# Kernel tuning notes

Measured on AMD Instinct MI355X. Metric: run time of the kernel, lower is better.

The kernel has to match this reference:

```python
import jax, jax.numpy as jnp
import numpy as np


def _lstm_scan(xs, K, R, b, units):
    """Keras-style LSTM over time-major xs [T,B,F].
    Gate order i,f,g,o; recurrent_activation=sigmoid; activation=swish
    (applied to candidate g AND to cell state in h = o*swish(c))."""
    B = xs.shape[1]
    h0 = jnp.zeros((B, units), xs.dtype)
    c0 = jnp.zeros((B, units), xs.dtype)

    def step(carry, xt):
        h, c = carry
        z = xt @ K + h @ R + b  # [B, 4U]
        i, f, g, o = jnp.split(z, 4, axis=-1)
        i = jax.nn.sigmoid(i)
        f = jax.nn.sigmoid(f)
        g = jax.nn.swish(g)
        o = jax.nn.sigmoid(o)
        c = f * c + i * g
        h = o * jax.nn.swish(c)
        return (h, c), h

    _, hs = jax.lax.scan(step, (h0, c0), xs)
    return hs  # [T,B,U]


def setup_inputs() -> dict:
    B, T, F, U = 32, 512, 64, 512
    key = jax.random.key(0)
    ks = jax.random.split(key, 7)
    s = 0.05  # RandomUniform-ish small init scale
    x = jax.random.normal(ks[0], (B, T, F), jnp.float32)
    Kf = jax.random.uniform(ks[1], (F, 4 * U), jnp.float32, -s, s)
    Rf = jax.random.uniform(ks[2], (U, 4 * U), jnp.float32, -s, s)
    bf = jax.random.uniform(ks[3], (4 * U,), jnp.float32, -s, s)
    Kb = jax.random.uniform(ks[4], (F, 4 * U), jnp.float32, -s, s)
    Rb = jax.random.uniform(ks[5], (U, 4 * U), jnp.float32, -s, s)
    bb = jax.random.uniform(ks[6], (4 * U,), jnp.float32, -s, s)
    return {"x": x, "Kf": Kf, "Rf": Rf, "bf": bf, "Kb": Kb, "Rb": Rb, "bb": bb}


def reference(x, Kf, Rf, bf, Kb, Rb, bb):
    U = Rf.shape[0]
    xs = jnp.swapaxes(x, 0, 1)  # [T,B,F] time-major
    h_fwd = _lstm_scan(xs, Kf, Rf, bf, U)                      # [T,B,U]
    h_bwd = _lstm_scan(xs[::-1], Kb, Rb, bb, U)[::-1]          # [T,B,U]
    out = jnp.concatenate([h_fwd, h_bwd], axis=-1)             # [T,B,2U]
    return jnp.swapaxes(out, 0, 1)                              # [B,T,2U]
```

## Files before the change

kernel.cpp:

```cpp
#include <hip/hip_runtime.h>
#include <hip/hip_cooperative_groups.h>
#include <hip/hip_bf16.h>

namespace cg = cooperative_groups;

#define T_STEPS 512
#define BATCH   32
#define FDIM    64
#define UDIM    512
#define NWG_DIR 32

typedef __attribute__((ext_vector_type(8))) __bf16 bf16x8;
typedef __attribute__((ext_vector_type(4))) float  f32x4;


__global__ __launch_bounds__(512, 2)
void lstm_bidir_kernel(const float* __restrict__ x,
                       const float* __restrict__ Kf, const float* __restrict__ Rf,
                       const float* __restrict__ bfp,
                       const float* __restrict__ Kb, const float* __restrict__ Rb,
                       const float* __restrict__ bbp,
                       float* __restrict__ out, float* __restrict__ ws)
{
    __shared__ __align__(16) unsigned char hsb[BATCH * 1024];
    __shared__ __align__(16) unsigned char xsb[2][BATCH * 128];
    __shared__ __align__(16) float zbuf[BATCH * 68];
    __shared__ float cbuf[512];
    __shared__ float bsh[64];

    const int tid = threadIdx.x;
    const int wg  = blockIdx.x;
    const int dir   = wg >> 5;
    const int slice = wg & 31;
    const int colbase = slice * 16;

    const float* Kg = dir ? Kb : Kf;
    const float* Rg = dir ? Rb : Rf;
    const float* bg = dir ? bbp : bfp;

    unsigned char* wsb = (unsigned char*)ws;
    int* cnt = (int*)(wsb + 131072);

    {
        int g = wg * 512 + tid;
        if (g < 8192) {
            ((unsigned int*)wsb)[g] = 0u;
        } else if (g < 16384) {
            ((unsigned int*)wsb)[g + 8192] = 0u;
        } else if (g < 16384 + 2 * T_STEPS) {
            cnt[g - 16384] = 0;
        }
    }
    if (tid < 64) bsh[tid] = bg[(tid >> 4) * 512 + colbase + (tid & 15)];
    cbuf[tid] = 0.f;

    const int lane = tid & 63;
    const int w    = tid >> 6;
    const int mt   = w >> 2;
    const int gate = w & 3;
    const int bn   = lane & 15;
    const int kq   = lane >> 4;
    const int gcol = gate * 512 + colbase + bn;

    bf16x8 breg[18];
    #pragma unroll
    for (int s = 0; s < 16; ++s) {
        const int k0 = s * 32 + kq * 8;
        bf16x8 v;
        #pragma unroll
        for (int e = 0; e < 8; ++e)
            v[e] = (__bf16)Rg[(size_t)(k0 + e) * 2048 + gcol];
        breg[s] = v;
    }
    #pragma unroll
    for (int s = 0; s < 2; ++s) {
        const int k0 = s * 32 + kq * 8;
        bf16x8 v;
        #pragma unroll
        for (int e = 0; e < 8; ++e)
            v[e] = (__bf16)Kg[(size_t)(k0 + e) * 2048 + gcol];
        breg[16 + s] = v;
    }

    {
        const int t0 = dir ? (T_STEPS - 1) : 0;
        if (tid < 256) {
            int b = tid >> 3, m = tid & 7;
            const float4* xg = (const float4*)(x + (size_t)b * (T_STEPS * FDIM) + (size_t)t0 * FDIM + m * 8);
            float4 v0 = xg[0], v1 = xg[1];
            unsigned int p0 = ((unsigned int)__builtin_bit_cast(unsigned short, (__bf16)v0.x)) |
                              ((unsigned int)__builtin_bit_cast(unsigned short, (__bf16)v0.y) << 16);
            unsigned int p1 = ((unsigned int)__builtin_bit_cast(unsigned short, (__bf16)v0.z)) |
                              ((unsigned int)__builtin_bit_cast(unsigned short, (__bf16)v0.w) << 16);
            unsigned int p2 = ((unsigned int)__builtin_bit_cast(unsigned short, (__bf16)v1.x)) |
                              ((unsigned int)__builtin_bit_cast(unsigned short, (__bf16)v1.y) << 16);
            unsigned int p3 = ((unsigned int)__builtin_bit_cast(unsigned short, (__bf16)v1.z)) |
                              ((unsigned int)__builtin_bit_cast(unsigned short, (__bf16)v1.w) << 16);
            uint4 pk = make_uint4(p0, p1, p2, p3);
            *(uint4*)(xsb[0] + b * 128 + (m ^ (b & 7)) * 16) = pk;
        }
    }

    cg::grid_group grid = cg::this_grid();
    grid.sync();

    const int bb = tid >> 4;
    const int q  = tid & 15;
    float h_keep = 0.f;

    int p = 0;
    #pragma unroll 1
    for (int t = 0; t < T_STEPS; ++t) {
        if (t > 0) {
            const int txp = dir ? (T_STEPS - t) : (t - 1);
            out[(size_t)bb * (T_STEPS * 2 * UDIM) + (size_t)txp * (2 * UDIM)
                + dir * UDIM + colbase + q] = h_keep;
        }

        {
            const unsigned char* srcrow = wsb + (size_t)(dir * 2 + p) * 32768 + bb * 1024;
            const int inv = bb & 7;
            uint4 r0, r1, r2, r3;
            asm volatile("global_load_dwordx4 %0, %1, off sc0 sc1"
                         : "=&v"(r0) : "v"(srcrow + (q +  0) * 16) : "memory");
            asm volatile("global_load_dwordx4 %0, %1, off sc0 sc1"
                         : "=&v"(r1) : "v"(srcrow + (q + 16) * 16) : "memory");
            asm volatile("global_load_dwordx4 %0, %1, off sc0 sc1"
                         : "=&v"(r2) : "v"(srcrow + (q + 32) * 16) : "memory");
            asm volatile("global_load_dwordx4 %0, %1, off sc0 sc1"
                         : "=&v"(r3) : "v"(srcrow + (q + 48) * 16) : "memory");

            if (t + 1 < T_STEPS && tid < 256) {
                const int tn = dir ? (T_STEPS - 2 - t) : (t + 1);
                int b = tid >> 3, m = tid & 7;
                const float4* xg = (const float4*)(x + (size_t)b * (T_STEPS * FDIM) + (size_t)tn * FDIM + m * 8);
                float4 v0 = xg[0], v1 = xg[1];
                unsigned int p0 = ((unsigned int)__builtin_bit_cast(unsigned short, (__bf16)v0.x)) |
                                  ((unsigned int)__builtin_bit_cast(unsigned short, (__bf16)v0.y) << 16);
                unsigned int p1 = ((unsigned int)__builtin_bit_cast(unsigned short, (__bf16)v0.z)) |
                                  ((unsigned int)__builtin_bit_cast(unsigned short, (__bf16)v0.w) << 16);
                unsigned int p2 = ((unsigned int)__builtin_bit_cast(unsigned short, (__bf16)v1.x)) |
                                  ((unsigned int)__builtin_bit_cast(unsigned short, (__bf16)v1.y) << 16);
                unsigned int p3 = ((unsigned int)__builtin_bit_cast(unsigned short, (__bf16)v1.z)) |
                                  ((unsigned int)__builtin_bit_cast(unsigned short, (__bf16)v1.w) << 16);
                uint4 pk = make_uint4(p0, p1, p2, p3);
                *(uint4*)(xsb[(t + 1) & 1] + b * 128 + (m ^ (b & 7)) * 16) = pk;
            }

            asm volatile("s_waitcnt vmcnt(0)" ::: "memory");
            __builtin_amdgcn_sched_barrier(0);

            unsigned char* hrow = hsb + bb * 1024;
            *(uint4*)(hrow + (((q +  0) ^ inv) << 4)) = r0;
            *(uint4*)(hrow + (((q + 16) ^ inv) << 4)) = r1;
            *(uint4*)(hrow + (((q + 32) ^ inv) << 4)) = r2;
            *(uint4*)(hrow + (((q + 48) ^ inv) << 4)) = r3;
        }
        __syncthreads();

        f32x4 acc = {0.f, 0.f, 0.f, 0.f};
        {
            const int arow = mt * 16 + bn;
            const int inv  = arow & 7;
            const unsigned char* hrowA = hsb + arow * 1024;
            #pragma unroll
            for (int s = 0; s < 16; ++s) {
                int m = s * 4 + kq;
                bf16x8 a = *(const bf16x8*)(hrowA + ((m ^ inv) * 16));
                acc = __builtin_amdgcn_mfma_f32_16x16x32_bf16(a, breg[s], acc, 0, 0, 0);
            }
            const unsigned char* xrowA = xsb[t & 1] + arow * 128;
            #pragma unroll
            for (int s = 0; s < 2; ++s) {
                int m = s * 4 + kq;
                bf16x8 a = *(const bf16x8*)(xrowA + ((m ^ inv) * 16));
                acc = __builtin_amdgcn_mfma_f32_16x16x32_bf16(a, breg[16 + s], acc, 0, 0, 0);
            }
            const int zb = mt * 16 + kq * 4;
            #pragma unroll
            for (int j = 0; j < 4; ++j)
                zbuf[(zb + j) * 68 + gate * 16 + bn] = acc[j];
        }
        __syncthreads();

        {
            const float* zr = zbuf + bb * 68 + q;
            float zi = zr[0]  + bsh[q];
            float zf = zr[16] + bsh[16 + q];
            float zg = zr[32] + bsh[32 + q];
            float zo = zr[48] + bsh[48 + q];
            float gi = 1.f / (1.f + __expf(-zi));
            float gf = 1.f / (1.f + __expf(-zf));
            float gg = zg / (1.f + __expf(-zg));
            float go = 1.f / (1.f + __expf(-zo));
            float cv = gf * cbuf[tid] + gi * gg;
            cbuf[tid] = cv;
            float h  = go * (cv / (1.f + __expf(-cv)));
            h_keep = h;

            unsigned short hu = __builtin_bit_cast(unsigned short, (__bf16)h);
            int other = __shfl_xor((int)hu, 1);
            if ((q & 1) == 0) {
                unsigned int packed = (unsigned int)hu | ((unsigned int)(unsigned short)other << 16);
                unsigned int* dst = (unsigned int*)(wsb + (size_t)(dir * 2 + (p ^ 1)) * 32768);
                __hip_atomic_store(dst + bb * 256 + ((colbase + q) >> 1), packed,
                                   __ATOMIC_RELAXED, __HIP_MEMORY_SCOPE_AGENT);
            }
        }
        __syncthreads();

        if (t < T_STEPS - 1) {
            if (tid == 0) {
                asm volatile("s_waitcnt vmcnt(0)" ::: "memory");
                int* c0 = &cnt[dir * T_STEPS + t];
                __hip_atomic_fetch_add(c0, 1, __ATOMIC_RELAXED, __HIP_MEMORY_SCOPE_AGENT);
                while (__hip_atomic_load(c0, __ATOMIC_RELAXED, __HIP_MEMORY_SCOPE_AGENT) < NWG_DIR)
                    __builtin_amdgcn_s_sleep(1);
            }
            __syncthreads();
        }
        p ^= 1;
    }

    {
        const int txl = dir ? 0 : (T_STEPS - 1);
        out[(size_t)bb * (T_STEPS * 2 * UDIM) + (size_t)txl * (2 * UDIM)
            + dir * UDIM + colbase + q] = h_keep;
    }
}

extern "C" void kernel_launch(void* const* d_in, const int* in_sizes, int n_in,
                              void* d_out, int out_size, void* d_ws, size_t ws_size,
                              hipStream_t stream) {
    (void)in_sizes; (void)n_in; (void)out_size; (void)ws_size;
    const float* x  = (const float*)d_in[0];
    const float* Kf = (const float*)d_in[1];
    const float* Rf = (const float*)d_in[2];
    const float* bf = (const float*)d_in[3];
    const float* Kb = (const float*)d_in[4];
    const float* Rb = (const float*)d_in[5];
    const float* bb = (const float*)d_in[6];
    float* out = (float*)d_out;
    float* ws  = (float*)d_ws;

    void* args[] = {&x, &Kf, &Rf, &bf, &Kb, &Rb, &bb, &out, &ws};
    hipLaunchCooperativeKernel((const void*)lstm_bidir_kernel,
                               dim3(64), dim3(512), args, 0, stream);
}
```

Baseline: 1.580 ms.

## Replace per-step counter barrier with sentinel-flagged triple-buffered hidden state polling

Drops the per-timestep atomic counter barrier between the 32 workgroups of each direction. Instead, the hidden state lives in a three-slot ring buffer, and each slot is pre-filled with a 0xFFFFFFFF sentinel. Readers spin on the data itself until no sentinel remains, then reset their own columns of the slot two steps ahead to the sentinel. The x prefetch load is also issued before the polling loop so it overlaps. This removes a full block-wide syncthreads, the atomic round-trip and the sleep polling per step. The cost is repeated 4KB-per-row reloads while waiting, and correctness now relies on a bf16 pair never bit-matching the sentinel.

Result: faster. 1.453 ms (-8.0%).

```diff
diff --git a/kernel.cpp b/kernel.cpp
--- a/kernel.cpp
+++ b/kernel.cpp
@@ -9,6 +9,7 @@
 #define FDIM    64
 #define UDIM    512
 #define NWG_DIR 32
+#define SENT    0xFFFFFFFFu
 
 typedef __attribute__((ext_vector_type(8))) __bf16 bf16x8;
 typedef __attribute__((ext_vector_type(4))) float  f32x4;
@@ -39,17 +40,14 @@
     const float* bg = dir ? bbp : bfp;
 
     unsigned char* wsb = (unsigned char*)ws;
-    int* cnt = (int*)(wsb + 131072);
+    unsigned char* dirbase = wsb + (size_t)dir * 98304;
 
     {
         int g = wg * 512 + tid;
-        if (g < 8192) {
-            ((unsigned int*)wsb)[g] = 0u;
-        } else if (g < 16384) {
-            ((unsigned int*)wsb)[g + 8192] = 0u;
-        } else if (g < 16384 + 2 * T_STEPS) {
-            cnt[g - 16384] = 0;
-        }
+        ((unsigned int*)wsb)[g] = (((g >> 13) % 3) == 0) ? 0u : SENT;
+        int g2 = g + 32768;
+        if (g2 < 49152)
+            ((unsigned int*)wsb)[g2] = (((g2 >> 13) % 3) == 0) ? 0u : SENT;
     }
     if (tid < 64) bsh[tid] = bg[(tid >> 4) * 512 + colbase + (tid & 15)];
     cbuf[tid] = 0.f;
@@ -108,7 +106,6 @@
     const int q  = tid & 15;
     float h_keep = 0.f;
 
-    int p = 0;
     #pragma unroll 1
     for (int t = 0; t < T_STEPS; ++t) {
         if (t > 0) {
@@ -117,44 +114,63 @@
                 + dir * UDIM + colbase + q] = h_keep;
         }
 
-        {
-            const unsigned char* srcrow = wsb + (size_t)(dir * 2 + p) * 32768 + bb * 1024;
+        float4 xv0, xv1;
+        const bool xload = (t + 1 < T_STEPS) && (tid < 256);
+        const int bxr = tid >> 3, mx = tid & 7;
+        if (xload) {
+            const int tn = dir ? (T_STEPS - 2 - t) : (t + 1);
+            const float4* xg = (const float4*)(x + (size_t)bxr * (T_STEPS * FDIM) + (size_t)tn * FDIM + mx * 8);
+            xv0 = xg[0]; xv1 = xg[1];
+        }
+
+        uint4 r0, r1, r2, r3;
+        {
+            const unsigned char* srcrow = dirbase + (size_t)(t % 3) * 32768 + bb * 1024;
+            for (;;) {
+                asm volatile("global_load_dwordx4 %0, %1, off sc0 sc1"
+                             : "=&v"(r0) : "v"(srcrow + (q +  0) * 16) : "memory");
+                asm volatile("global_load_dwordx4 %0, %1, off sc0 sc1"
+                             : "=&v"(r1) : "v"(srcrow + (q + 16) * 16) : "memory");
+                asm volatile("global_load_dwordx4 %0, %1, off sc0 sc1"
+                             : "=&v"(r2) : "v"(srcrow + (q + 32) * 16) : "memory");
+                asm volatile("global_load_dwordx4 %0, %1, off sc0 sc1"
+                             : "=&v"(r3) : "v"(srcrow + (q + 48) * 16) : "memory");
+                asm volatile("s_waitcnt vmcnt(0)" ::: "memory");
+                __builtin_amdgcn_sched_barrier(0);
+                unsigned bad = (r0.x == SENT) | (r0.y == SENT) | (r0.z == SENT) | (r0.w == SENT)
+                             | (r1.x == SENT) | (r1.y == SENT) | (r1.z == SENT) | (r1.w == SENT)
+                             | (r2.x == SENT) | (r2.y == SENT) | (r2.z == SENT) | (r2.w == SENT)
+                             | (r3.x == SENT) | (r3.y == SENT) | (r3.z == SENT) | (r3.w == SENT);
+                if (!bad) break;
+            }
+        }
+
+        if (tid < 256) {
+            int prow = tid >> 3, pd = tid & 7;
+            unsigned int* pp = (unsigned int*)(dirbase + (size_t)((t + 2) % 3) * 32768
+                                               + prow * 1024 + colbase * 2) + pd;
+            __hip_atomic_store(pp, SENT, __ATOMIC_RELAXED, __HIP_MEMORY_SCOPE_AGENT);
+        }
+
+        {
             const int inv = bb & 7;
-            uint4 r0, r1, r2, r3;
-            asm volatile("global_load_dwordx4 %0, %1, off sc0 sc1"
-                         : "=&v"(r0) : "v"(srcrow + (q +  0) * 16) : "memory");
-            asm volatile("global_load_dwordx4 %0, %1, off sc0 sc1"
-                         : "=&v"(r1) : "v"(srcrow + (q + 16) * 16) : "memory");
-            asm volatile("global_load_dwordx4 %0, %1, off sc0 sc1"
-                         : "=&v"(r2) : "v"(srcrow + (q + 32) * 16) : "memory");
-            asm volatile("global_load_dwordx4 %0, %1, off sc0 sc1"
-                         : "=&v"(r3) : "v"(srcrow + (q + 48) * 16) : "memory");
-
-            if (t + 1 < T_STEPS && tid < 256) {
-                const int tn = dir ? (T_STEPS - 2 - t) : (t + 1);
-                int b = tid >> 3, m = tid & 7;
-                const float4* xg = (const float4*)(x + (size_t)b * (T_STEPS * FDIM) + (size_t)tn * FDIM + m * 8);
-                float4 v0 = xg[0], v1 = xg[1];
-                unsigned int p0 = ((unsigned int)__builtin_bit_cast(unsigned short, (__bf16)v0.x)) |
-                                  ((unsigned int)__builtin_bit_cast(unsigned short, (__bf16)v0.y) << 16);
-                unsigned int p1 = ((unsigned int)__builtin_bit_cast(unsigned short, (__bf16)v0.z)) |
-                                  ((unsigned int)__builtin_bit_cast(unsigned short, (__bf16)v0.w) << 16);
-                unsigned int p2 = ((unsigned int)__builtin_bit_cast(unsigned short, (__bf16)v1.x)) |
-                                  ((unsigned int)__builtin_bit_cast(unsigned short, (__bf16)v1.y) << 16);
-                unsigned int p3 = ((unsigned int)__builtin_bit_cast(unsigned short, (__bf16)v1.z)) |
-                                  ((unsigned int)__builtin_bit_cast(unsigned short, (__bf16)v1.w) << 16);
-                uint4 pk = make_uint4(p0, p1, p2, p3);
-                *(uint4*)(xsb[(t + 1) & 1] + b * 128 + (m ^ (b & 7)) * 16) = pk;
-            }
-
-            asm volatile("s_waitcnt vmcnt(0)" ::: "memory");
-            __builtin_amdgcn_sched_barrier(0);
-
             unsigned char* hrow = hsb + bb * 1024;
             *(uint4*)(hrow + (((q +  0) ^ inv) << 4)) = r0;
             *(uint4*)(hrow + (((q + 16) ^ inv) << 4)) = r1;
             *(uint4*)(hrow + (((q + 32) ^ inv) << 4)) = r2;
             *(uint4*)(hrow + (((q + 48) ^ inv) << 4)) = r3;
+        }
+        if (xload) {
+            unsigned int p0 = ((unsigned int)__builtin_bit_cast(unsigned short, (__bf16)xv0.x)) |
+                              ((unsigned int)__builtin_bit_cast(unsigned short, (__bf16)xv0.y) << 16);
+            unsigned int p1 = ((unsigned int)__builtin_bit_cast(unsigned short, (__bf16)xv0.z)) |
+                              ((unsigned int)__builtin_bit_cast(unsigned short, (__bf16)xv0.w) << 16);
+            unsigned int p2 = ((unsigned int)__builtin_bit_cast(unsigned short, (__bf16)xv1.x)) |
+                              ((unsigned int)__builtin_bit_cast(unsigned short, (__bf16)xv1.y) << 16);
+            unsigned int p3 = ((unsigned int)__builtin_bit_cast(unsigned short, (__bf16)xv1.z)) |
+                              ((unsigned int)__builtin_bit_cast(unsigned short, (__bf16)xv1.w) << 16);
+            uint4 pk = make_uint4(p0, p1, p2, p3);
+            *(uint4*)(xsb[(t + 1) & 1] + bxr * 128 + ((mx ^ (bxr & 7)) * 16)) = pk;
         }
         __syncthreads();
 
@@ -200,26 +216,14 @@
 
             unsigned short hu = __builtin_bit_cast(unsigned short, (__bf16)h);
             int other = __shfl_xor((int)hu, 1);
+            asm volatile("s_waitcnt vmcnt(0)" ::: "memory");
             if ((q & 1) == 0) {
                 unsigned int packed = (unsigned int)hu | ((unsigned int)(unsigned short)other << 16);
-                unsigned int* dst = (unsigned int*)(wsb + (size_t)(dir * 2 + (p ^ 1)) * 32768);
-                __hip_atomic_store(dst + bb * 256 + ((colbase + q) >> 1), packed,
-                                   __ATOMIC_RELAXED, __HIP_MEMORY_SCOPE_AGENT);
-            }
-        }
-        __syncthreads();
-
-        if (t < T_STEPS - 1) {
-            if (tid == 0) {
-                asm volatile("s_waitcnt vmcnt(0)" ::: "memory");
-                int* c0 = &cnt[dir * T_STEPS + t];
-                __hip_atomic_fetch_add(c0, 1, __ATOMIC_RELAXED, __HIP_MEMORY_SCOPE_AGENT);
-                while (__hip_atomic_load(c0, __ATOMIC_RELAXED, __HIP_MEMORY_SCOPE_AGENT) < NWG_DIR)
-                    __builtin_amdgcn_s_sleep(1);
-            }
-            __syncthreads();
-        }
-        p ^= 1;
+                unsigned int* dst = (unsigned int*)(dirbase + (size_t)((t + 1) % 3) * 32768)
+                                    + bb * 256 + ((colbase + q) >> 1);
+                __hip_atomic_store(dst, packed, __ATOMIC_RELAXED, __HIP_MEMORY_SCOPE_AGENT);
+            }
+        }
     }
 
     {
```
